# Performance work log

Measured on AMD Instinct MI355X. Metric: run time of the kernel, lower is better.

## Reference

```python
import jax, jax.numpy as jnp
import numpy as np

B, S, R, H = 64, 256, 196, 1024

def setup_inputs() -> dict:
    key = jax.random.key(0)
    ks = jax.random.split(key, 12)
    s = 0.02
    return {
        "dns_feature": jax.random.normal(ks[0], (B, S, H), jnp.float32),
        "img_features": jax.random.normal(ks[1], (B, R, H), jnp.float32),
        "W_dns1": jax.random.normal(ks[2], (H, H), jnp.float32) * s,
        "b_dns1": jax.random.normal(ks[3], (H,), jnp.float32) * s,
        "W_img1": jax.random.normal(ks[4], (H, H), jnp.float32) * s,
        "w_att1": jax.random.normal(ks[5], (2 * H,), jnp.float32) * s,
        "b_att1": jax.random.normal(ks[6], (), jnp.float32) * s,
        "W_dns2": jax.random.normal(ks[7], (H, H), jnp.float32) * s,
        "W_img2": jax.random.normal(ks[8], (H, H), jnp.float32) * s,
        "b_img2": jax.random.normal(ks[9], (H,), jnp.float32) * s,
        "w_att2": jax.random.normal(ks[10], (2 * H,), jnp.float32) * s,
        "b_att2": jax.random.normal(ks[11], (), jnp.float32) * s,
    }

def reference(dns_feature, img_features, W_dns1, b_dns1, W_img1, w_att1, b_att1,
              W_dns2, W_img2, b_img2, w_att2, b_att2):
    h = W_dns1.shape[0]
    # --- stage 1: textual attention (img queries over dns positions) ---
    # tanh(concat([img_proj, dns_proj])) then 2H->1 linear decomposes into
    # per-side dot products + broadcast add (repeat is position-wise redundant).
    dns_p1 = jnp.tanh(jnp.einsum('bsh,oh->bso', dns_feature, W_dns1) + b_dns1)  # (B,S,H)
    img_p1 = jnp.tanh(jnp.einsum('brh,oh->bro', img_features, W_img1))          # (B,R,H)
    s_img = img_p1 @ w_att1[:h]   # (B,R)  concat order: [img, dns]
    s_dns = dns_p1 @ w_att1[h:]   # (B,S)
    scores1 = s_img[:, :, None] + s_dns[:, None, :] + b_att1                    # (B,R,S)
    a1 = jax.nn.softmax(scores1, axis=-1)
    att_dns = jnp.einsum('brs,bsh->brh', a1, dns_feature)                       # (B,R,H)
    # --- stage 2: visual attention (attended-dns queries over img regions) ---
    dns_p2 = jnp.tanh(jnp.einsum('brh,oh->bro', att_dns, W_dns2))               # (B,R,H)
    img_p2 = jnp.tanh(jnp.einsum('brh,oh->bro', img_features, W_img2) + b_img2) # (B,R,H)
    t_dns = dns_p2 @ w_att2[:h]   # (B,R)  concat order: [dns, img]
    t_img = img_p2 @ w_att2[h:]   # (B,R)
    scores2 = t_dns[:, :, None] + t_img[:, None, :] + b_att2                    # (B,R,R)
    a2 = jax.nn.softmax(scores2, axis=-1)
    att_img = jnp.einsum('bij,bjh->bih', a2, img_features)                      # (B,R,H)
    return att_img, att_dns
```

## Files before the change

kernel.cpp:

```cpp
#include <hip/hip_runtime.h>

#define Hdim 1024
#define BB 64
#define SS 256
#define RR 196
#define MD (BB * SS)
#define MI (BB * RR)

typedef __attribute__((ext_vector_type(8))) short short8;
typedef __attribute__((ext_vector_type(4))) float floatx4;
typedef unsigned short us;

__device__ __forceinline__ unsigned short f2bf(float f) {
  unsigned int u = __float_as_uint(f);
  unsigned int r = 0x7FFFu + ((u >> 16) & 1u);
  return (unsigned short)((u + r) >> 16);
}

__device__ __forceinline__ float fast_tanh(float x) {
  x = fminf(15.f, fmaxf(-15.f, x));
  float e = __expf(2.f * x);
  return (e - 1.f) / (e + 1.f);
}

#define GLOAD16(g, l) __builtin_amdgcn_global_load_lds( \
    (const __attribute__((address_space(1))) unsigned int*)(g), \
    (__attribute__((address_space(3))) unsigned int*)(l), 16, 0, 0)

__global__ __launch_bounds__(256) void prep_kernel(
    const float4* __restrict__ dns, const float4* __restrict__ img,
    const float4* __restrict__ Wd1, const float4* __restrict__ Wi2,
    uint4* __restrict__ dns_bf, uint4* __restrict__ img_bf,
    uint4* __restrict__ wd1_bf, uint4* __restrict__ wi2_bf,
    float4* __restrict__ scz)
{
  constexpr int N0 = (MD * Hdim) / 8;
  constexpr int N1 = N0 + (MI * Hdim) / 8;
  constexpr int N2 = N1 + (Hdim * Hdim) / 8;
  constexpr int N3 = N2 + (Hdim * Hdim) / 8;
  constexpr int N4 = N3 + (MD + MI) / 8;
  const int stride = gridDim.x * 256;
  for (int i = blockIdx.x * 256 + threadIdx.x; i < N4; i += stride) {
    if (i < N3) {
      const float4* src; uint4* dst; int li;
      if (i < N0)      { src = dns; dst = dns_bf; li = i; }
      else if (i < N1) { src = img; dst = img_bf; li = i - N0; }
      else if (i < N2) { src = Wd1; dst = wd1_bf; li = i - N1; }
      else             { src = Wi2; dst = wi2_bf; li = i - N2; }
      const float4 a = src[2 * li];
      const float4 b = src[2 * li + 1];
      uint4 o;
      o.x = (unsigned)f2bf(a.x) | ((unsigned)f2bf(a.y) << 16);
      o.y = (unsigned)f2bf(a.z) | ((unsigned)f2bf(a.w) << 16);
      o.z = (unsigned)f2bf(b.x) | ((unsigned)f2bf(b.y) << 16);
      o.w = (unsigned)f2bf(b.z) | ((unsigned)f2bf(b.w) << 16);
      dst[li] = o;
    } else {
      const int li = i - N3;
      const float4 z4 = {0.f, 0.f, 0.f, 0.f};
      scz[2 * li]     = z4;
      scz[2 * li + 1] = z4;
    }
  }
}

__global__ __launch_bounds__(256) void gemm_score_bf2(
    const us* __restrict__ X1, const us* __restrict__ W1,
    const float* __restrict__ bias1, const float* __restrict__ v1, float* sc1,
    const us* __restrict__ X2, const us* __restrict__ W2,
    const float* __restrict__ bias2, const float* __restrict__ v2, float* sc2)
{
  __shared__ us Ash[128 * 64];
  __shared__ us Bsh[128 * 64];

  const int q  = gridDim.x >> 3;
  const int wg = (blockIdx.x & 7) * q + (blockIdx.x >> 3);

  const us* Xb; const us* Wb; const float* bias; const float* vatt; float* scores;
  int mt, nt;
  if (wg < (MD / 128) * 8) {
    Xb = X1; Wb = W1; bias = bias1; vatt = v1; scores = sc1;
    mt = wg >> 3; nt = wg & 7;
  } else {
    const int w2 = wg - (MD / 128) * 8;
    Xb = X2; Wb = W2; bias = bias2; vatt = v2; scores = sc2;
    mt = w2 >> 3; nt = w2 & 7;
  }
  const long m0 = (long)mt * 128;
  const long n0 = (long)nt * 128;

  const int tid  = threadIdx.x;
  const int lane = tid & 63;
  const int wave = tid >> 6;
  const int waveM = (wave >> 1) * 64;
  const int waveN = (wave & 1) * 64;

  const int rowSub  = lane >> 3;
  const int srcColE = (((lane & 7) ^ rowSub)) * 8;

  const us* gA[4]; const us* gB[4];
  const us* lA[4]; const us* lB[4];
  #pragma unroll
  for (int c = 0; c < 4; ++c) {
    const int r = (wave * 4 + c) * 8 + rowSub;
    gA[c] = Xb + (m0 + r) * Hdim + srcColE;
    gB[c] = Wb + (n0 + r) * Hdim + srcColE;
    lA[c] = Ash + (wave * 4 + c) * 512 + lane * 8;
    lB[c] = Bsh + (wave * 4 + c) * 512 + lane * 8;
  }

  floatx4 acc[4][4];
  #pragma unroll
  for (int i = 0; i < 4; ++i)
    #pragma unroll
    for (int j = 0; j < 4; ++j)
      acc[i][j] = (floatx4){0.f, 0.f, 0.f, 0.f};

  const int frow = lane & 15;
  const int g    = lane >> 4;
  const int sw   = frow & 7;

  for (int k0 = 0; k0 < Hdim; k0 += 64) {
    __syncthreads();
    #pragma unroll
    for (int c = 0; c < 4; ++c) {
      GLOAD16(gA[c] + k0, lA[c]);
      GLOAD16(gB[c] + k0, lB[c]);
    }
    __syncthreads();
    #pragma unroll
    for (int ks = 0; ks < 2; ++ks) {
      const int slot = ((ks * 4 + g) ^ sw) * 8;
      short8 afr[4], bfr[4];
      #pragma unroll
      for (int mf = 0; mf < 4; ++mf)
        afr[mf] = *(const short8*)(Ash + (waveM + mf * 16 + frow) * 64 + slot);
      #pragma unroll
      for (int nf = 0; nf < 4; ++nf)
        bfr[nf] = *(const short8*)(Bsh + (waveN + nf * 16 + frow) * 64 + slot);
      #pragma unroll
      for (int mf = 0; mf < 4; ++mf)
        #pragma unroll
        for (int nf = 0; nf < 4; ++nf)
          acc[mf][nf] = __builtin_amdgcn_mfma_f32_16x16x32_bf16(afr[mf], bfr[nf], acc[mf][nf], 0, 0, 0);
    }
  }

  const int rgrp = lane >> 4;
  #pragma unroll
  for (int mf = 0; mf < 4; ++mf) {
    float part[4] = {0.f, 0.f, 0.f, 0.f};
    #pragma unroll
    for (int nf = 0; nf < 4; ++nf) {
      const int n = (int)n0 + waveN + nf * 16 + (lane & 15);
      const float bi = bias[n];
      const float vv = vatt[n];
      #pragma unroll
      for (int j = 0; j < 4; ++j)
        part[j] += fast_tanh(acc[mf][nf][j] + bi) * vv;
    }
    #pragma unroll
    for (int j = 0; j < 4; ++j) {
      float s = part[j];
      s += __shfl_xor(s, 1);
      s += __shfl_xor(s, 2);
      s += __shfl_xor(s, 4);
      s += __shfl_xor(s, 8);
      if ((lane & 15) == 0) {
        const int m = (int)m0 + waveM + mf * 16 + rgrp * 4 + j;
        atomicAdd(&scores[m], s);
      }
    }
  }
}

__global__ __launch_bounds__(256) void attend_bcast(
    const float* __restrict__ sc_d, const us* __restrict__ dns_bf,
    const float* __restrict__ sc_i, const us* __restrict__ img_bf,
    float* __restrict__ out)
{
  __shared__ float p[256];
  __shared__ float red[256];
  const int b  = blockIdx.x;
  const int h0 = blockIdx.y * 512;
  const int z  = blockIdx.z;
  const int L  = z ? RR : SS;
  const float* scores = z ? sc_i : sc_d;
  const us*    feat   = z ? img_bf : dns_bf;
  float* outp = out + (z ? (size_t)0 : (size_t)BB * RR * Hdim);
  const int t = threadIdx.x;

  const float sc = (t < L) ? scores[b * L + t] : -1e30f;
  red[t] = sc;
  __syncthreads();
  for (int off = 128; off > 0; off >>= 1) {
    if (t < off) red[t] = fmaxf(red[t], red[t + off]);
    __syncthreads();
  }
  const float mx = red[0];
  __syncthreads();
  const float e = (t < L) ? __expf(sc - mx) : 0.f;
  red[t] = e;
  __syncthreads();
  for (int off = 128; off > 0; off >>= 1) {
    if (t < off) red[t] += red[t + off];
    __syncthreads();
  }
  p[t] = e / red[0];
  __syncthreads();

  const int h = h0 + 2 * t;
  const us* fb = feat + (size_t)b * L * Hdim + h;
  float a0 = 0.f, a1 = 0.f;
  #pragma unroll 8
  for (int s = 0; s < L; ++s) {
    const unsigned u = *(const unsigned*)(fb + (size_t)s * Hdim);
    const float f0 = __uint_as_float(u << 16);
    const float f1 = __uint_as_float(u & 0xffff0000u);
    a0 += p[s] * f0;
    a1 += p[s] * f1;
  }

  float* ob = outp + (size_t)b * RR * Hdim + h;
  const float2 v = make_float2(a0, a1);
  #pragma unroll 4
  for (int r = 0; r < RR; ++r)
    *(float2*)(ob + (size_t)r * Hdim) = v;
}

__global__ __launch_bounds__(256) void gemm_score(
    const float* __restrict__ X, const float* __restrict__ W,
    const float* __restrict__ bias, const float* __restrict__ vatt,
    float* __restrict__ scores)
{
  __shared__ us Ash[128 * 32];
  __shared__ us Bsh[128 * 32];
  const int tid  = threadIdx.x;
  const int lane = tid & 63;
  const int wave = tid >> 6;
  const int waveM = (wave >> 1) * 64;
  const int waveN = (wave & 1) * 64;
  const long m0 = (long)blockIdx.x * 128;
  const long n0 = (long)blockIdx.y * 128;
  const int ldRow   = tid >> 3;
  const int ldChunk = (tid & 7) * 4;

  floatx4 acc[4][4];
  #pragma unroll
  for (int i = 0; i < 4; ++i)
    #pragma unroll
    for (int j = 0; j < 4; ++j)
      acc[i][j] = (floatx4){0.f, 0.f, 0.f, 0.f};

  const int frow = lane & 15;
  const int fk   = (lane >> 4) * 8;

  for (int k0 = 0; k0 < Hdim; k0 += 32) {
    __syncthreads();
    #pragma unroll
    for (int p = 0; p < 4; ++p) {
      const int r = ldRow + p * 32;
      const float4 av = *(const float4*)&X[(m0 + r) * Hdim + k0 + ldChunk];
      const float4 bv = *(const float4*)&W[(n0 + r) * Hdim + k0 + ldChunk];
      uint2 ap, bp;
      ap.x = (unsigned)f2bf(av.x) | ((unsigned)f2bf(av.y) << 16);
      ap.y = (unsigned)f2bf(av.z) | ((unsigned)f2bf(av.w) << 16);
      bp.x = (unsigned)f2bf(bv.x) | ((unsigned)f2bf(bv.y) << 16);
      bp.y = (unsigned)f2bf(bv.z) | ((unsigned)f2bf(bv.w) << 16);
      *(uint2*)&Ash[r * 32 + ldChunk] = ap;
      *(uint2*)&Bsh[r * 32 + ldChunk] = bp;
    }
    __syncthreads();
    short8 afr[4], bfr[4];
    #pragma unroll
    for (int mf = 0; mf < 4; ++mf)
      afr[mf] = *(const short8*)&Ash[(waveM + mf * 16 + frow) * 32 + fk];
    #pragma unroll
    for (int nf = 0; nf < 4; ++nf)
      bfr[nf] = *(const short8*)&Bsh[(waveN + nf * 16 + frow) * 32 + fk];
    #pragma unroll
    for (int mf = 0; mf < 4; ++mf)
      #pragma unroll
      for (int nf = 0; nf < 4; ++nf)
        acc[mf][nf] = __builtin_amdgcn_mfma_f32_16x16x32_bf16(afr[mf], bfr[nf], acc[mf][nf], 0, 0, 0);
  }

  const int rgrp = lane >> 4;
  #pragma unroll
  for (int mf = 0; mf < 4; ++mf) {
    float part[4] = {0.f, 0.f, 0.f, 0.f};
    #pragma unroll
    for (int nf = 0; nf < 4; ++nf) {
      const int n = (int)n0 + waveN + nf * 16 + (lane & 15);
      const float bi = bias[n];
      const float vv = vatt[n];
      #pragma unroll
      for (int j = 0; j < 4; ++j)
        part[j] += fast_tanh(acc[mf][nf][j] + bi) * vv;
    }
    #pragma unroll
    for (int j = 0; j < 4; ++j) {
      float s = part[j];
      s += __shfl_xor(s, 1);
      s += __shfl_xor(s, 2);
      s += __shfl_xor(s, 4);
      s += __shfl_xor(s, 8);
      if ((lane & 15) == 0) {
        const int m = (int)m0 + waveM + mf * 16 + rgrp * 4 + j;
        atomicAdd(&scores[m], s);
      }
    }
  }
}

template <int L>
__global__ __launch_bounds__(256) void softmax_attend(
    const float* __restrict__ scores, const float* __restrict__ feat,
    float* __restrict__ attended)
{
  __shared__ float p[256];
  __shared__ float red[256];
  const int b  = blockIdx.x;
  const int h0 = blockIdx.y * 256;
  const int t  = threadIdx.x;

  const float sc = (t < L) ? scores[b * L + t] : -1e30f;
  red[t] = sc;
  __syncthreads();
  for (int off = 128; off > 0; off >>= 1) {
    if (t < off) red[t] = fmaxf(red[t], red[t + off]);
    __syncthreads();
  }
  const float mx = red[0];
  __syncthreads();
  const float e = (t < L) ? __expf(sc - mx) : 0.f;
  red[t] = e;
  __syncthreads();
  for (int off = 128; off > 0; off >>= 1) {
    if (t < off) red[t] += red[t + off];
    __syncthreads();
  }
  p[t] = e / red[0];
  __syncthreads();

  const int h = h0 + t;
  const float* fb = feat + (size_t)b * L * Hdim + h;
  float acc = 0.f;
  #pragma unroll 4
  for (int s = 0; s < L; ++s)
    acc += p[s] * fb[(size_t)s * Hdim];
  attended[b * Hdim + h] = acc;
}

__global__ __launch_bounds__(256) void broadcast_out(
    const float4* __restrict__ att_img, const float4* __restrict__ att_dns,
    float4* __restrict__ out)
{
  const int H4 = Hdim / 4;
  const long region_sz = (long)BB * RR * H4;
  const long total = 2 * region_sz;
  for (long i = (long)blockIdx.x * blockDim.x + threadIdx.x; i < total;
       i += (long)gridDim.x * blockDim.x) {
    const int region = (i >= region_sz);
    const long rem = i - (long)region * region_sz;
    const int b  = (int)(rem / (RR * H4));
    const int h4 = (int)(rem % H4);
    const float4* src = region ? att_dns : att_img;
    out[i] = src[b * H4 + h4];
  }
}

extern "C" void kernel_launch(void* const* d_in, const int* in_sizes, int n_in,
                              void* d_out, int out_size, void* d_ws, size_t ws_size,
                              hipStream_t stream) {
  const float* dns    = (const float*)d_in[0];
  const float* img    = (const float*)d_in[1];
  const float* W_dns1 = (const float*)d_in[2];
  const float* b_dns1 = (const float*)d_in[3];
  const float* w_att1 = (const float*)d_in[5];
  const float* W_img2 = (const float*)d_in[8];
  const float* b_img2 = (const float*)d_in[9];
  const float* w_att2 = (const float*)d_in[10];

  const size_t dnsB = (size_t)MD * Hdim * 2;
  const size_t imgB = (size_t)MI * Hdim * 2;
  const size_t wB   = (size_t)Hdim * Hdim * 2;
  const size_t scoresB = (16384 + 12544) * sizeof(float);
  const size_t need = dnsB + imgB + 2 * wB + scoresB;

  dim3 blk(256);

  if (ws_size >= need) {
    char* cur = (char*)d_ws;
    us* dns_bf = (us*)cur; cur += dnsB;
    us* img_bf = (us*)cur; cur += imgB;
    us* Wd1_bf = (us*)cur; cur += wB;
    us* Wi2_bf = (us*)cur; cur += wB;
    float* s_dns = (float*)cur;
    float* t_img = s_dns + 16384;

    prep_kernel<<<2048, blk, 0, stream>>>(
        (const float4*)dns, (const float4*)img,
        (const float4*)W_dns1, (const float4*)W_img2,
        (uint4*)dns_bf, (uint4*)img_bf, (uint4*)Wd1_bf, (uint4*)Wi2_bf,
        (float4*)s_dns);

    gemm_score_bf2<<<dim3((MD / 128 + MI / 128) * 8), blk, 0, stream>>>(
        dns_bf, Wd1_bf, b_dns1, w_att1 + Hdim, s_dns,
        img_bf, Wi2_bf, b_img2, w_att2 + Hdim, t_img);

    attend_bcast<<<dim3(BB, Hdim / 512, 2), blk, 0, stream>>>(
        s_dns, dns_bf, t_img, img_bf, (float*)d_out);
  } else {
    float* ws    = (float*)d_ws;
    float* s_dns = ws;
    float* t_img = ws + 16384;
    float* att_d = ws + 16384 + 12544;
    float* att_i = att_d + BB * Hdim;

    hipMemsetAsync(s_dns, 0, (16384 + 12544) * sizeof(float), stream);

    gemm_score<<<dim3(MD / 128, Hdim / 128), blk, 0, stream>>>(
        dns, W_dns1, b_dns1, w_att1 + Hdim, s_dns);
    gemm_score<<<dim3(MI / 128, Hdim / 128), blk, 0, stream>>>(
        img, W_img2, b_img2, w_att2 + Hdim, t_img);

    softmax_attend<SS><<<dim3(BB, Hdim / 256), blk, 0, stream>>>(s_dns, dns, att_d);
    softmax_attend<RR><<<dim3(BB, Hdim / 256), blk, 0, stream>>>(t_img, img, att_i);

    broadcast_out<<<2048, blk, 0, stream>>>((const float4*)att_i, (const float4*)att_d,
                                            (float4*)d_out);
  }
}
```

Before: 167.2 us.

## Rewrite score GEMM as 256x256 tile, 8-wave, double-buffered LDS pipeline

Replaces the 128x128 single-buffered bf16 MFMA GEMM with a 256x256 tile computed by 8 waves (512 threads). It double-buffers LDS so the next K-slice's A and B loads are issued between MFMA phases, synchronised by raw barriers and s_setprio. The XCD block remapping now handles grid sizes that are not a multiple of 8. The larger tile halves global traffic per FLOP and overlaps loads with compute, at the cost of 128KB of LDS, higher register pressure and fewer workgroups (tail imbalance).

```diff
diff --git a/kernel.cpp b/kernel.cpp
--- a/kernel.cpp
+++ b/kernel.cpp
@@ -26,6 +26,8 @@
 #define GLOAD16(g, l) __builtin_amdgcn_global_load_lds( \
     (const __attribute__((address_space(1))) unsigned int*)(g), \
     (__attribute__((address_space(3))) unsigned int*)(l), 16, 0, 0)
+
+#define MEMFENCE asm volatile("" ::: "memory")
 
 __global__ __launch_bounds__(256) void prep_kernel(
     const float4* __restrict__ dns, const float4* __restrict__ img,
@@ -64,54 +66,57 @@
   }
 }
 
-__global__ __launch_bounds__(256) void gemm_score_bf2(
+#define NB1 ((MD / 256) * 4)
+#define NB2 ((MI / 256) * 4)
+
+__global__ __launch_bounds__(512, 2) void gemm_score_8p(
     const us* __restrict__ X1, const us* __restrict__ W1,
     const float* __restrict__ bias1, const float* __restrict__ v1, float* sc1,
     const us* __restrict__ X2, const us* __restrict__ W2,
     const float* __restrict__ bias2, const float* __restrict__ v2, float* sc2)
 {
-  __shared__ us Ash[128 * 64];
-  __shared__ us Bsh[128 * 64];
-
-  const int q  = gridDim.x >> 3;
-  const int wg = (blockIdx.x & 7) * q + (blockIdx.x >> 3);
+  __shared__ us LDS[65536];
+
+  const int nwg = gridDim.x;
+  const int q = nwg >> 3, rr = nwg & 7;
+  const int xcd = blockIdx.x & 7, idx = blockIdx.x >> 3;
+  const int wg = (xcd < rr ? xcd * (q + 1) : rr * (q + 1) + (xcd - rr) * q) + idx;
 
   const us* Xb; const us* Wb; const float* bias; const float* vatt; float* scores;
   int mt, nt;
-  if (wg < (MD / 128) * 8) {
+  if (wg < NB1) {
     Xb = X1; Wb = W1; bias = bias1; vatt = v1; scores = sc1;
-    mt = wg >> 3; nt = wg & 7;
+    mt = wg >> 2; nt = wg & 3;
   } else {
-    const int w2 = wg - (MD / 128) * 8;
+    const int w2 = wg - NB1;
     Xb = X2; Wb = W2; bias = bias2; vatt = v2; scores = sc2;
-    mt = w2 >> 3; nt = w2 & 7;
-  }
-  const long m0 = (long)mt * 128;
-  const long n0 = (long)nt * 128;
+    mt = w2 >> 2; nt = w2 & 3;
+  }
+  const long m0 = (long)mt * 256;
+  const long n0 = (long)nt * 256;
 
   const int tid  = threadIdx.x;
   const int lane = tid & 63;
-  const int wave = tid >> 6;
-  const int waveM = (wave >> 1) * 64;
-  const int waveN = (wave & 1) * 64;
-
-  const int rowSub  = lane >> 3;
-  const int srcColE = (((lane & 7) ^ rowSub)) * 8;
-
-  const us* gA[4]; const us* gB[4];
-  const us* lA[4]; const us* lB[4];
+  const int w    = tid >> 6;
+  const int wm   = w >> 2;
+  const int wn   = w & 3;
+
+  const int srow = lane >> 3;
+  const int scol = ((lane & 7) ^ srow) * 8;
+  const us* gA = Xb + (m0 + w * 8 + srow) * Hdim + scol;
+  const us* gB = Wb + (n0 + w * 8 + srow) * Hdim + scol;
+  const int ldl = (w * 64 + lane) * 8;
+
+#define STAGE_A(d, h, kk) do { \
+    GLOAD16(gA + ((h) * 128 + 0) * Hdim + (kk),  &LDS[(d) * 16384 + (h) * 8192 + 0    + ldl]); \
+    GLOAD16(gA + ((h) * 128 + 64) * Hdim + (kk), &LDS[(d) * 16384 + (h) * 8192 + 4096 + ldl]); } while (0)
+#define STAGE_B(d, h, kk) do { \
+    GLOAD16(gB + ((h) * 128 + 0) * Hdim + (kk),  &LDS[32768 + (d) * 16384 + (h) * 8192 + 0    + ldl]); \
+    GLOAD16(gB + ((h) * 128 + 64) * Hdim + (kk), &LDS[32768 + (d) * 16384 + (h) * 8192 + 4096 + ldl]); } while (0)
+
+  floatx4 acc[8][4];
   #pragma unroll
-  for (int c = 0; c < 4; ++c) {
-    const int r = (wave * 4 + c) * 8 + rowSub;
-    gA[c] = Xb + (m0 + r) * Hdim + srcColE;
-    gB[c] = Wb + (n0 + r) * Hdim + srcColE;
-    lA[c] = Ash + (wave * 4 + c) * 512 + lane * 8;
-    lB[c] = Bsh + (wave * 4 + c) * 512 + lane * 8;
-  }
-
-  floatx4 acc[4][4];
-  #pragma unroll
-  for (int i = 0; i < 4; ++i)
+  for (int i = 0; i < 8; ++i)
     #pragma unroll
     for (int j = 0; j < 4; ++j)
       acc[i][j] = (floatx4){0.f, 0.f, 0.f, 0.f};
@@ -119,40 +124,82 @@
   const int frow = lane & 15;
   const int g    = lane >> 4;
   const int sw   = frow & 7;
-
-  for (int k0 = 0; k0 < Hdim; k0 += 64) {
-    __syncthreads();
-    #pragma unroll
-    for (int c = 0; c < 4; ++c) {
-      GLOAD16(gA[c] + k0, lA[c]);
-      GLOAD16(gB[c] + k0, lB[c]);
-    }
-    __syncthreads();
-    #pragma unroll
-    for (int ks = 0; ks < 2; ++ks) {
-      const int slot = ((ks * 4 + g) ^ sw) * 8;
-      short8 afr[4], bfr[4];
-      #pragma unroll
-      for (int mf = 0; mf < 4; ++mf)
-        afr[mf] = *(const short8*)(Ash + (waveM + mf * 16 + frow) * 64 + slot);
+  const int aRow = wm * 8192 + frow * 64;
+  const int bRow = (wn >> 1) * 8192 + ((wn & 1) * 64 + frow) * 64;
+
+  STAGE_A(0, 0, 0); STAGE_A(0, 1, 0); STAGE_B(0, 0, 0); STAGE_B(0, 1, 0);
+  asm volatile("s_waitcnt vmcnt(0)" ::: "memory");
+  MEMFENCE; __builtin_amdgcn_s_barrier(); MEMFENCE;
+
+  #pragma unroll 1
+  for (int T = 0; T < 16; ++T) {
+    const int d   = T & 1;
+    const int kk1 = (T + 1) * 64;
+    const int Ab  = d * 16384 + aRow;
+    const int Bb  = 32768 + d * 16384 + bRow;
+    const int s0  = (g ^ sw) * 8;
+    const int s1  = ((4 + g) ^ sw) * 8;
+    short8 a[4], b0[4], b1[4];
+
+    if (T < 15) { STAGE_A(d ^ 1, 0, kk1); STAGE_A(d ^ 1, 1, kk1); }
+    #pragma unroll
+    for (int mf = 0; mf < 4; ++mf) a[mf] = *(const short8*)&LDS[Ab + mf * 1024 + s0];
+    #pragma unroll
+    for (int nf = 0; nf < 4; ++nf) b0[nf] = *(const short8*)&LDS[Bb + nf * 1024 + s0];
+    __builtin_amdgcn_s_setprio(1);
+    #pragma unroll
+    for (int mf = 0; mf < 4; ++mf)
       #pragma unroll
       for (int nf = 0; nf < 4; ++nf)
-        bfr[nf] = *(const short8*)(Bsh + (waveN + nf * 16 + frow) * 64 + slot);
-      #pragma unroll
-      for (int mf = 0; mf < 4; ++mf)
-        #pragma unroll
-        for (int nf = 0; nf < 4; ++nf)
-          acc[mf][nf] = __builtin_amdgcn_mfma_f32_16x16x32_bf16(afr[mf], bfr[nf], acc[mf][nf], 0, 0, 0);
-    }
+        acc[mf][nf] = __builtin_amdgcn_mfma_f32_16x16x32_bf16(a[mf], b0[nf], acc[mf][nf], 0, 0, 0);
+    __builtin_amdgcn_s_setprio(0);
+    MEMFENCE; __builtin_amdgcn_s_barrier(); MEMFENCE;
+
+    if (T < 15) { STAGE_B(d ^ 1, 0, kk1); STAGE_B(d ^ 1, 1, kk1); }
+    #pragma unroll
+    for (int mf = 0; mf < 4; ++mf) a[mf] = *(const short8*)&LDS[Ab + (mf + 4) * 1024 + s0];
+    __builtin_amdgcn_s_setprio(1);
+    #pragma unroll
+    for (int mf = 0; mf < 4; ++mf)
+      #pragma unroll
+      for (int nf = 0; nf < 4; ++nf)
+        acc[mf + 4][nf] = __builtin_amdgcn_mfma_f32_16x16x32_bf16(a[mf], b0[nf], acc[mf + 4][nf], 0, 0, 0);
+    __builtin_amdgcn_s_setprio(0);
+    MEMFENCE; __builtin_amdgcn_s_barrier(); MEMFENCE;
+
+    #pragma unroll
+    for (int mf = 0; mf < 4; ++mf) a[mf] = *(const short8*)&LDS[Ab + mf * 1024 + s1];
+    #pragma unroll
+    for (int nf = 0; nf < 4; ++nf) b1[nf] = *(const short8*)&LDS[Bb + nf * 1024 + s1];
+    __builtin_amdgcn_s_setprio(1);
+    #pragma unroll
+    for (int mf = 0; mf < 4; ++mf)
+      #pragma unroll
+      for (int nf = 0; nf < 4; ++nf)
+        acc[mf][nf] = __builtin_amdgcn_mfma_f32_16x16x32_bf16(a[mf], b1[nf], acc[mf][nf], 0, 0, 0);
+    __builtin_amdgcn_s_setprio(0);
+    MEMFENCE; __builtin_amdgcn_s_barrier(); MEMFENCE;
+
+    #pragma unroll
+    for (int mf = 0; mf < 4; ++mf) a[mf] = *(const short8*)&LDS[Ab + (mf + 4) * 1024 + s1];
+    __builtin_amdgcn_s_setprio(1);
+    #pragma unroll
+    for (int mf = 0; mf < 4; ++mf)
+      #pragma unroll
+      for (int nf = 0; nf < 4; ++nf)
+        acc[mf + 4][nf] = __builtin_amdgcn_mfma_f32_16x16x32_bf16(a[mf], b1[nf], acc[mf + 4][nf], 0, 0, 0);
+    __builtin_amdgcn_s_setprio(0);
+    asm volatile("s_waitcnt vmcnt(0)" ::: "memory");
+    MEMFENCE; __builtin_amdgcn_s_barrier(); MEMFENCE;
   }
 
   const int rgrp = lane >> 4;
   #pragma unroll
-  for (int mf = 0; mf < 4; ++mf) {
+  for (int mf = 0; mf < 8; ++mf) {
     float part[4] = {0.f, 0.f, 0.f, 0.f};
     #pragma unroll
     for (int nf = 0; nf < 4; ++nf) {
-      const int n = (int)n0 + waveN + nf * 16 + (lane & 15);
+      const int n = (int)n0 + wn * 64 + nf * 16 + (lane & 15);
       const float bi = bias[n];
       const float vv = vatt[n];
       #pragma unroll
@@ -167,11 +214,13 @@
       s += __shfl_xor(s, 4);
       s += __shfl_xor(s, 8);
       if ((lane & 15) == 0) {
-        const int m = (int)m0 + waveM + mf * 16 + rgrp * 4 + j;
+        const int m = (int)m0 + wm * 128 + mf * 16 + rgrp * 4 + j;
         atomicAdd(&scores[m], s);
       }
     }
   }
+#undef STAGE_A
+#undef STAGE_B
 }
 
 __global__ __launch_bounds__(256) void attend_bcast(
@@ -405,7 +454,7 @@
         (uint4*)dns_bf, (uint4*)img_bf, (uint4*)Wd1_bf, (uint4*)Wi2_bf,
         (float4*)s_dns);
 
-    gemm_score_bf2<<<dim3((MD / 128 + MI / 128) * 8), blk, 0, stream>>>(
+    gemm_score_8p<<<dim3(NB1 + NB2), dim3(512), 0, stream>>>(
         dns_bf, Wd1_bf, b_dns1, w_att1 + Hdim, s_dns,
         img_bf, Wi2_bf, b_img2, w_att2 + Hdim, t_img);
 
```

Result: faster. 154.6 us (-7.5%).
